# Kernel tuning notes

Measured on AMD Instinct MI355X. Metric: run time of the kernel, lower is better.

## Reference

```python
import jax, jax.numpy as jnp
import numpy as np


def setup_inputs() -> dict:
    key = jax.random.key(0)
    k1, k2 = jax.random.split(key)
    bsz, n_views, d = 4096, 2, 512
    features = jax.random.normal(k1, (bsz, n_views, d), dtype=jnp.float32)
    labels = jax.random.randint(k2, (bsz,), 0, 100)
    return {"features": features, "labels": labels}


def reference(features, labels):
    # Faithful vectorization of Fourdloss.forward (contrast_mode='all').
    bsz, n_views, d = features.shape
    N = bsz * n_views
    # torch.cat(torch.unbind(features, dim=1), dim=0): view-major stacking
    cf = jnp.transpose(features, (1, 0, 2)).reshape(N, d)  # contrast == anchor feature
    lab = jnp.tile(labels, n_views)                        # labels2[i] = labels[i % bsz]
    same = lab[:, None] == lab[None, :]                    # [N, N]
    neg = ~same                                            # mask2
    negf = neg.astype(jnp.float32)
    # positive mask with diagonal removed (mask * logits_mask)
    pos_mask = same.astype(jnp.float32) * (1.0 - jnp.eye(N, dtype=jnp.float32))

    # pairwise dot products with the hardcoded 0.035 temperature
    D = (cf @ cf.T) / 0.035                                # [N, N], D[m, j] = c_m . a_j / 0.035

    # Inner loop over j: over rows m with labels2[m] != labels2[j],
    # S[j] = sum_m exp(D[m, j] - max_m D[m, j])
    maxd = jnp.max(jnp.where(neg, D, -jnp.inf), axis=0)    # [N], per-column masked max
    z = jnp.where(neg, D - maxd[None, :], 0.0)             # safe: masked entries -> exp(0)*0
    S = jnp.sum(jnp.exp(z) * negf, axis=0)                 # [N]

    # Outer loop over i: sum S[j] over all j that are negatives of i; k = count
    num = negf @ S                                         # negtive_dot_negtive_sum
    negcount = negf.sum(axis=1)                            # negtivesum (k)
    x = num / negcount                                     # [N] (repeated across columns in torch)
    log_prob = -jnp.log(x + 1e-12)                         # constant per row

    pos_count = pos_mask.sum(axis=1)
    mask_sum = jnp.where(pos_count == 0, 1.0, pos_count)
    # (mask * log_prob).sum(1) == log_prob * pos_count since log_prob is row-constant
    pos_logits = -(pos_count * log_prob) / mask_sum
    loss = pos_logits.reshape(n_views, bsz).mean()
    return loss
```

## Files before the change

kernel.cpp:

```cpp
#include <hip/hip_runtime.h>

typedef unsigned short u16;
typedef unsigned int u32;
typedef __attribute__((ext_vector_type(8))) short bfrag;
typedef __attribute__((ext_vector_type(4))) float facc;

#define N 8192
#define DIM 512
#define BM 128
#define BK 64
#define NTILE 2080
#define NPART 64
#define NCLS 100

#if __has_builtin(__builtin_amdgcn_exp2f)
#define EXP2(x) __builtin_amdgcn_exp2f(x)
#else
#define EXP2(x) exp2f(x)
#endif

__device__ __forceinline__ u16 f2bf(float f) {
  u32 u = __float_as_uint(f);
  u32 r = u + 0x7fffu + ((u >> 16) & 1u);
  return (u16)(r >> 16);
}
__device__ __forceinline__ float bf2f(u16 h) {
  return __uint_as_float(((u32)h) << 16);
}

__global__ void prep_kernel(const float* __restrict__ F, u16* __restrict__ Ahi,
                            u16* __restrict__ Alo, float* __restrict__ classSum,
                            int* __restrict__ classCnt)
{
  const float sc = sqrtf(1.4426950408889634f / 0.035f);
  int idx = (blockIdx.x * 256 + threadIdx.x) * 4;
  float4 x = *(const float4*)(F + idx);
  float v[4] = {x.x * sc, x.y * sc, x.z * sc, x.w * sc};
  u16 h[4], l[4];
#pragma unroll
  for (int i = 0; i < 4; ++i) {
    h[i] = f2bf(v[i]);
    l[i] = f2bf(v[i] - bf2f(h[i]));
  }
  *(ushort4*)(Ahi + idx) = make_ushort4(h[0], h[1], h[2], h[3]);
  *(ushort4*)(Alo + idx) = make_ushort4(l[0], l[1], l[2], l[3]);
  if (blockIdx.x == 0 && threadIdx.x < NCLS) {
    classSum[threadIdx.x] = 0.f;
    classCnt[threadIdx.x] = 0;
  }
}

__device__ __forceinline__ void stage16(const u16* g, u16* l) {
  __builtin_amdgcn_global_load_lds((const __attribute__((address_space(1))) void*)g,
                                   (__attribute__((address_space(3))) void*)l, 16, 0, 0);
}

__device__ __forceinline__ void mergeMS(float& m, float& s, float m2, float s2) {
  float M = fmaxf(m, m2);
  s = s * EXP2(m - M) + s2 * EXP2(m2 - M);
  m = M;
}

__global__ __launch_bounds__(256, 2) void gram_flash(
    const u16* __restrict__ Ahi, const u16* __restrict__ Alo,
    const int* __restrict__ labels,
    float* __restrict__ m_part, float* __restrict__ s_part)
{
  __shared__ __align__(16) u16 lds[4 * BM * BK];
  u16* lds_ahi = lds;
  u16* lds_alo = lds + BM * BK;
  u16* lds_bhi = lds + 2 * BM * BK;
  u16* lds_blo = lds + 3 * BM * BK;

  const int tid = threadIdx.x;
  const int wave = tid >> 6;
  const int lane = tid & 63;
  const int wr = wave >> 1, wc = wave & 1;
  const int l15 = lane & 15, lg = lane >> 4;

  const int t = blockIdx.x;
  int I = (int)((129.0f - sqrtf(16641.0f - 8.0f * (float)t)) * 0.5f);
  while ((I + 1) * 64 - ((I + 1) * I) / 2 <= t) ++I;
  while (I * 64 - (I * (I - 1)) / 2 > t) --I;
  const int J = I + (t - (I * 64 - (I * (I - 1)) / 2));
  const int i0 = I * BM;
  const int j0 = J * BM;

  u32 lr[4];
#pragma unroll
  for (int mi = 0; mi < 4; ++mi) {
    u32 pk = 0;
#pragma unroll
    for (int rg = 0; rg < 4; ++rg) {
      int r = i0 + wr * 64 + mi * 16 + lg * 4 + rg;
      pk |= ((u32)labels[r >> 1] & 0xffu) << (8 * rg);
    }
    lr[mi] = pk;
  }
  int lc[4];
#pragma unroll
  for (int ni = 0; ni < 4; ++ni)
    lc[ni] = labels[(j0 + wc * 64 + ni * 16 + l15) >> 1];

  facc acc[4][4];
#pragma unroll
  for (int a = 0; a < 4; ++a)
#pragma unroll
    for (int b = 0; b < 4; ++b)
      acc[a][b] = (facc){0.f, 0.f, 0.f, 0.f};

  for (int kk = 0; kk < DIM; kk += BK) {
    __syncthreads();
#pragma unroll
    for (int q = 0; q < 4; ++q) {
      const int ci = (wave * 4 + q) * 64 + lane;
      const int row = ci >> 3;
      const int cp = ci & 7;
      const int cg = cp ^ (row & 7);
      const size_t goffA = (size_t)(i0 + row) * DIM + kk + cg * 8;
      const size_t goffB = (size_t)(j0 + row) * DIM + kk + cg * 8;
      const int lbase = (wave * 4 + q) * 512;
      stage16(Ahi + goffA, lds_ahi + lbase);
      stage16(Alo + goffA, lds_alo + lbase);
      stage16(Ahi + goffB, lds_bhi + lbase);
      stage16(Alo + goffB, lds_blo + lbase);
    }
    asm volatile("s_waitcnt vmcnt(0)" ::: "memory");
    __syncthreads();

#pragma unroll
    for (int k2 = 0; k2 < 2; ++k2) {
      bfrag fah[4], fal[4], fbh[4], fbl[4];
#pragma unroll
      for (int mi = 0; mi < 4; ++mi) {
        const int row = wr * 64 + mi * 16 + l15;
        const int cc = (k2 * 4 + lg) ^ (row & 7);
        const int off = row * 64 + cc * 8;
        fah[mi] = *(const bfrag*)(lds_ahi + off);
        fal[mi] = *(const bfrag*)(lds_alo + off);
      }
#pragma unroll
      for (int ni = 0; ni < 4; ++ni) {
        const int row = wc * 64 + ni * 16 + l15;
        const int cc = (k2 * 4 + lg) ^ (row & 7);
        const int off = row * 64 + cc * 8;
        fbh[ni] = *(const bfrag*)(lds_bhi + off);
        fbl[ni] = *(const bfrag*)(lds_blo + off);
      }
#pragma unroll
      for (int mi = 0; mi < 4; ++mi)
#pragma unroll
        for (int ni = 0; ni < 4; ++ni)
          acc[mi][ni] = __builtin_amdgcn_mfma_f32_16x16x32_bf16(fah[mi], fbh[ni], acc[mi][ni], 0, 0, 0);
#pragma unroll
      for (int mi = 0; mi < 4; ++mi)
#pragma unroll
        for (int ni = 0; ni < 4; ++ni)
          acc[mi][ni] = __builtin_amdgcn_mfma_f32_16x16x32_bf16(fah[mi], fbl[ni], acc[mi][ni], 0, 0, 0);
#pragma unroll
      for (int mi = 0; mi < 4; ++mi)
#pragma unroll
        for (int ni = 0; ni < 4; ++ni)
          acc[mi][ni] = __builtin_amdgcn_mfma_f32_16x16x32_bf16(fal[mi], fbh[ni], acc[mi][ni], 0, 0, 0);
    }
  }

#pragma unroll
  for (int mi = 0; mi < 4; ++mi)
#pragma unroll
    for (int rg = 0; rg < 4; ++rg) {
      const int labr = (int)((lr[mi] >> (8 * rg)) & 0xffu);
#pragma unroll
      for (int ni = 0; ni < 4; ++ni)
        if (labr == lc[ni]) acc[mi][ni][rg] = -1e30f;
    }

  float rm[16], rs[16];
#pragma unroll
  for (int mi = 0; mi < 4; ++mi)
#pragma unroll
    for (int rg = 0; rg < 4; ++rg) {
      const int si = mi * 4 + rg;
      float m = -1e20f;
#pragma unroll
      for (int ni = 0; ni < 4; ++ni) m = fmaxf(m, acc[mi][ni][rg]);
      float s = 0.f;
#pragma unroll
      for (int ni = 0; ni < 4; ++ni) s += EXP2(acc[mi][ni][rg] - m);
      rm[si] = m; rs[si] = s;
    }
#pragma unroll
  for (int st = 1; st <= 8; st <<= 1)
#pragma unroll
    for (int si = 0; si < 16; ++si)
      mergeMS(rm[si], rs[si], __shfl_xor(rm[si], st, 64), __shfl_xor(rs[si], st, 64));

  float cm[4], cs[4];
#pragma unroll
  for (int ni = 0; ni < 4; ++ni) {
    float m = -1e20f;
#pragma unroll
    for (int mi = 0; mi < 4; ++mi)
#pragma unroll
      for (int rg = 0; rg < 4; ++rg) m = fmaxf(m, acc[mi][ni][rg]);
    float s = 0.f;
#pragma unroll
    for (int mi = 0; mi < 4; ++mi)
#pragma unroll
      for (int rg = 0; rg < 4; ++rg) s += EXP2(acc[mi][ni][rg] - m);
    cm[ni] = m; cs[ni] = s;
  }
#pragma unroll
  for (int st = 16; st <= 32; st <<= 1)
#pragma unroll
    for (int ni = 0; ni < 4; ++ni)
      mergeMS(cm[ni], cs[ni], __shfl_xor(cm[ni], st, 64), __shfl_xor(cs[ni], st, 64));

  float* buf = (float*)lds;
  float* RM = buf;
  float* RS = buf + 256;
  float* CM = buf + 512;
  float* CS = buf + 768;

  __syncthreads();
  if (l15 == 0) {
#pragma unroll
    for (int mi = 0; mi < 4; ++mi)
#pragma unroll
      for (int rg = 0; rg < 4; ++rg) {
        const int idx = wr * 64 + mi * 16 + lg * 4 + rg;
        RM[wc * 128 + idx] = rm[mi * 4 + rg];
        RS[wc * 128 + idx] = rs[mi * 4 + rg];
      }
  }
  if (lg == 0 && I != J) {
#pragma unroll
    for (int ni = 0; ni < 4; ++ni) {
      const int c = wc * 64 + ni * 16 + l15;
      CM[wr * 128 + c] = cm[ni];
      CS[wr * 128 + c] = cs[ni];
    }
  }
  __syncthreads();

  if (tid < 128) {
    float m = RM[tid], s = RS[tid];
    mergeMS(m, s, RM[128 + tid], RS[128 + tid]);
    m_part[(size_t)J * N + i0 + tid] = m;
    s_part[(size_t)J * N + i0 + tid] = s;
  } else if (I != J) {
    const int c = tid - 128;
    float m = CM[c], s = CS[c];
    mergeMS(m, s, CM[128 + c], CS[128 + c]);
    m_part[(size_t)I * N + j0 + c] = m;
    s_part[(size_t)I * N + j0 + c] = s;
  }
}

__global__ void combine_kernel(const float* __restrict__ m_part,
                               const float* __restrict__ s_part,
                               const int* __restrict__ labels,
                               float* __restrict__ classSum,
                               int* __restrict__ classCnt)
{
  int j = blockIdx.x * 256 + threadIdx.x;
  float M = -1e20f;
  for (int p = 0; p < NPART; ++p) M = fmaxf(M, m_part[p * N + j]);
  float S = 0.f;
  for (int p = 0; p < NPART; ++p)
    S += s_part[p * N + j] * EXP2(m_part[p * N + j] - M);
  int c = labels[j >> 1];
  atomicAdd(&classSum[c], S);
  atomicAdd(&classCnt[c], 1);
}

__global__ void final_kernel(const float* __restrict__ classSum,
                             const int* __restrict__ classCnt,
                             float* __restrict__ out)
{
  __shared__ float red[128];
  int t = threadIdx.x;
  float total = 0.f;
  for (int c = 0; c < NCLS; ++c) total += classSum[c];
  float term = 0.f;
  if (t < NCLS) {
    int cnt = classCnt[t];
    if (cnt > 0) {
      float x = (total - classSum[t]) / (float)(N - cnt) + 1e-12f;
      term = (float)cnt * logf(x);
    }
  }
  red[t] = term;
  __syncthreads();
  for (int s = 64; s > 0; s >>= 1) {
    if (t < s) red[t] += red[t + s];
    __syncthreads();
  }
  if (t == 0) out[0] = red[0] / (float)N;
}

extern "C" void kernel_launch(void* const* d_in, const int* in_sizes, int n_in,
                              void* d_out, int out_size, void* d_ws, size_t ws_size,
                              hipStream_t stream)
{
  (void)in_sizes; (void)n_in; (void)out_size; (void)ws_size;
  const float* F = (const float*)d_in[0];
  const int* labels = (const int*)d_in[1];
  float* out = (float*)d_out;

  char* ws = (char*)d_ws;
  u16* Ahi = (u16*)ws;
  u16* Alo = (u16*)(ws + (size_t)N * DIM * 2);
  float* m_part = (float*)(ws + (size_t)N * DIM * 4);
  float* s_part = m_part + (size_t)NPART * N;
  float* classSum = s_part + (size_t)NPART * N;
  int* classCnt = (int*)(classSum + NCLS);

  prep_kernel<<<(N * DIM) / 1024, 256, 0, stream>>>(F, Ahi, Alo, classSum, classCnt);
  gram_flash<<<NTILE, 256, 0, stream>>>(Ahi, Alo, labels, m_part, s_part);
  combine_kernel<<<N / 256, 256, 0, stream>>>(m_part, s_part, labels, classSum, classCnt);
  final_kernel<<<1, 128, 0, stream>>>(classSum, classCnt, out);
}
```

Measured before the change: 221.5 us.

## Halve K-tile, raise occupancy, and remap triangular tiles into XCD-local supertiles

The K tile shrinks from 64 to 32, which halves the LDS footprint. Launch bounds are raised to target 4 blocks per CU. The triangular tile index is remapped into 8x8 supertiles, with block IDs interleaved by 8 so that each XCD works on neighbouring tiles and shares their rows in L2. The LDS swizzle is rewritten to pack two rows per 64-element line. The costs are twice as many sync and wait rounds over K and more register pressure under the tighter launch bounds.

```diff
diff --git a/kernel.cpp b/kernel.cpp
--- a/kernel.cpp
+++ b/kernel.cpp
@@ -8,10 +8,11 @@
 #define N 8192
 #define DIM 512
 #define BM 128
-#define BK 64
+#define BK 32
 #define NTILE 2080
 #define NPART 64
 #define NCLS 100
+#define TPX 260
 
 #if __has_builtin(__builtin_amdgcn_exp2f)
 #define EXP2(x) __builtin_amdgcn_exp2f(x)
@@ -61,7 +62,7 @@
   m = M;
 }
 
-__global__ __launch_bounds__(256, 2) void gram_flash(
+__global__ __launch_bounds__(256, 4) void gram_flash(
     const u16* __restrict__ Ahi, const u16* __restrict__ Alo,
     const int* __restrict__ labels,
     float* __restrict__ m_part, float* __restrict__ s_part)
@@ -78,11 +79,27 @@
   const int wr = wave >> 1, wc = wave & 1;
   const int l15 = lane & 15, lg = lane >> 4;
 
-  const int t = blockIdx.x;
-  int I = (int)((129.0f - sqrtf(16641.0f - 8.0f * (float)t)) * 0.5f);
-  while ((I + 1) * 64 - ((I + 1) * I) / 2 <= t) ++I;
-  while (I * 64 - (I * (I - 1)) / 2 > t) --I;
-  const int J = I + (t - (I * 64 - (I * (I - 1)) / 2));
+  const int t = (blockIdx.x & 7) * TPX + (blockIdx.x >> 3);
+  int SI = 0, base = 0;
+  for (;; ++SI) {
+    int rowcnt = 36 + (7 - SI) * 64;
+    if (t < base + rowcnt) break;
+    base += rowcnt;
+  }
+  const int r = t - base;
+  int SJ, li, lj;
+  if (r < 36) {
+    SJ = SI;
+    int a = 0, cum = 0;
+    for (;; ++a) { if (r < cum + (8 - a)) break; cum += 8 - a; }
+    li = a; lj = a + (r - cum);
+  } else {
+    int rr = r - 36;
+    SJ = SI + 1 + (rr >> 6);
+    li = (rr & 63) >> 3;
+    lj = rr & 7;
+  }
+  const int I = SI * 8 + li, J = SJ * 8 + lj;
   const int i0 = I * BM;
   const int j0 = J * BM;
 
@@ -92,8 +109,8 @@
     u32 pk = 0;
 #pragma unroll
     for (int rg = 0; rg < 4; ++rg) {
-      int r = i0 + wr * 64 + mi * 16 + lg * 4 + rg;
-      pk |= ((u32)labels[r >> 1] & 0xffu) << (8 * rg);
+      int rr2 = i0 + wr * 64 + mi * 16 + lg * 4 + rg;
+      pk |= ((u32)labels[rr2 >> 1] & 0xffu) << (8 * rg);
     }
     lr[mi] = pk;
   }
@@ -112,14 +129,16 @@
   for (int kk = 0; kk < DIM; kk += BK) {
     __syncthreads();
 #pragma unroll
-    for (int q = 0; q < 4; ++q) {
-      const int ci = (wave * 4 + q) * 64 + lane;
-      const int row = ci >> 3;
-      const int cp = ci & 7;
-      const int cg = cp ^ (row & 7);
-      const size_t goffA = (size_t)(i0 + row) * DIM + kk + cg * 8;
-      const size_t goffB = (size_t)(j0 + row) * DIM + kk + cg * 8;
-      const int lbase = (wave * 4 + q) * 512;
+    for (int q = 0; q < 2; ++q) {
+      const int ci = (wave * 2 + q) * 64 + lane;
+      const int L = ci >> 3;
+      const int sc2 = ci & 7;
+      const int cb = sc2 ^ (L & 7);
+      const int row = L * 2 + (cb >> 2);
+      const int kc = cb & 3;
+      const size_t goffA = (size_t)(i0 + row) * DIM + kk + kc * 8;
+      const size_t goffB = (size_t)(j0 + row) * DIM + kk + kc * 8;
+      const int lbase = (wave * 2 + q) * 512;
       stage16(Ahi + goffA, lds_ahi + lbase);
       stage16(Alo + goffA, lds_alo + lbase);
       stage16(Ahi + goffB, lds_bhi + lbase);
@@ -128,41 +147,40 @@
     asm volatile("s_waitcnt vmcnt(0)" ::: "memory");
     __syncthreads();
 
-#pragma unroll
-    for (int k2 = 0; k2 < 2; ++k2) {
-      bfrag fah[4], fal[4], fbh[4], fbl[4];
-#pragma unroll
-      for (int mi = 0; mi < 4; ++mi) {
-        const int row = wr * 64 + mi * 16 + l15;
-        const int cc = (k2 * 4 + lg) ^ (row & 7);
-        const int off = row * 64 + cc * 8;
-        fah[mi] = *(const bfrag*)(lds_ahi + off);
-        fal[mi] = *(const bfrag*)(lds_alo + off);
-      }
-#pragma unroll
-      for (int ni = 0; ni < 4; ++ni) {
-        const int row = wc * 64 + ni * 16 + l15;
-        const int cc = (k2 * 4 + lg) ^ (row & 7);
-        const int off = row * 64 + cc * 8;
-        fbh[ni] = *(const bfrag*)(lds_bhi + off);
-        fbl[ni] = *(const bfrag*)(lds_blo + off);
-      }
-#pragma unroll
-      for (int mi = 0; mi < 4; ++mi)
-#pragma unroll
-        for (int ni = 0; ni < 4; ++ni)
-          acc[mi][ni] = __builtin_amdgcn_mfma_f32_16x16x32_bf16(fah[mi], fbh[ni], acc[mi][ni], 0, 0, 0);
-#pragma unroll
-      for (int mi = 0; mi < 4; ++mi)
-#pragma unroll
-        for (int ni = 0; ni < 4; ++ni)
-          acc[mi][ni] = __builtin_amdgcn_mfma_f32_16x16x32_bf16(fah[mi], fbl[ni], acc[mi][ni], 0, 0, 0);
-#pragma unroll
-      for (int mi = 0; mi < 4; ++mi)
-#pragma unroll
-        for (int ni = 0; ni < 4; ++ni)
-          acc[mi][ni] = __builtin_amdgcn_mfma_f32_16x16x32_bf16(fal[mi], fbh[ni], acc[mi][ni], 0, 0, 0);
-    }
+    bfrag fah[4], fal[4], fbh[4], fbl[4];
+#pragma unroll
+    for (int mi = 0; mi < 4; ++mi) {
+      const int row = wr * 64 + mi * 16 + l15;
+      const int L = row >> 1;
+      const int cb = ((row & 1) << 2) | lg;
+      const int off = L * 64 + (cb ^ (L & 7)) * 8;
+      fah[mi] = *(const bfrag*)(lds_ahi + off);
+      fal[mi] = *(const bfrag*)(lds_alo + off);
+    }
+#pragma unroll
+    for (int ni = 0; ni < 4; ++ni) {
+      const int row = wc * 64 + ni * 16 + l15;
+      const int L = row >> 1;
+      const int cb = ((row & 1) << 2) | lg;
+      const int off = L * 64 + (cb ^ (L & 7)) * 8;
+      fbh[ni] = *(const bfrag*)(lds_bhi + off);
+      fbl[ni] = *(const bfrag*)(lds_blo + off);
+    }
+#pragma unroll
+    for (int mi = 0; mi < 4; ++mi)
+#pragma unroll
+      for (int ni = 0; ni < 4; ++ni)
+        acc[mi][ni] = __builtin_amdgcn_mfma_f32_16x16x32_bf16(fah[mi], fbh[ni], acc[mi][ni], 0, 0, 0);
+#pragma unroll
+    for (int mi = 0; mi < 4; ++mi)
+#pragma unroll
+      for (int ni = 0; ni < 4; ++ni)
+        acc[mi][ni] = __builtin_amdgcn_mfma_f32_16x16x32_bf16(fah[mi], fbl[ni], acc[mi][ni], 0, 0, 0);
+#pragma unroll
+    for (int mi = 0; mi < 4; ++mi)
+#pragma unroll
+      for (int ni = 0; ni < 4; ++ni)
+        acc[mi][ni] = __builtin_amdgcn_mfma_f32_16x16x32_bf16(fal[mi], fbh[ni], acc[mi][ni], 0, 0, 0);
   }
 
 #pragma unroll
```

Result: no change. 220.4 us (-0.5%).

## Swizzle triangular tile order into XCD-local supertiles and parallelize combine

Applied to the files above, without the earlier changes.

Remaps the block index of the triangular Gram tile grid so that consecutive blocks on each of the 8 XCDs (blockIdx & 7) walk 8x8 supertiles. Operand row panels then get reused in each XCD's L2 instead of being refetched. The combine kernel now splits the 64 partials across 4 waves per column group, merges them with an online max/sum in shared memory, and launches 4x more blocks for more parallelism. The cost is extra index arithmetic with small loops per block.

```diff
diff --git a/kernel.cpp b/kernel.cpp
--- a/kernel.cpp
+++ b/kernel.cpp
@@ -12,6 +12,7 @@
 #define NTILE 2080
 #define NPART 64
 #define NCLS 100
+#define TPX 260
 
 #if __has_builtin(__builtin_amdgcn_exp2f)
 #define EXP2(x) __builtin_amdgcn_exp2f(x)
@@ -78,11 +79,27 @@
   const int wr = wave >> 1, wc = wave & 1;
   const int l15 = lane & 15, lg = lane >> 4;
 
-  const int t = blockIdx.x;
-  int I = (int)((129.0f - sqrtf(16641.0f - 8.0f * (float)t)) * 0.5f);
-  while ((I + 1) * 64 - ((I + 1) * I) / 2 <= t) ++I;
-  while (I * 64 - (I * (I - 1)) / 2 > t) --I;
-  const int J = I + (t - (I * 64 - (I * (I - 1)) / 2));
+  const int t = (blockIdx.x & 7) * TPX + (blockIdx.x >> 3);
+  int SI = 0, base = 0;
+  for (;; ++SI) {
+    int rowcnt = 36 + (7 - SI) * 64;
+    if (t < base + rowcnt) break;
+    base += rowcnt;
+  }
+  const int r = t - base;
+  int SJ, li, lj;
+  if (r < 36) {
+    SJ = SI;
+    int a = 0, cum = 0;
+    for (;; ++a) { if (r < cum + (8 - a)) break; cum += 8 - a; }
+    li = a; lj = a + (r - cum);
+  } else {
+    int rr = r - 36;
+    SJ = SI + 1 + (rr >> 6);
+    li = (rr & 63) >> 3;
+    lj = rr & 7;
+  }
+  const int I = SI * 8 + li, J = SJ * 8 + lj;
   const int i0 = I * BM;
   const int j0 = J * BM;
 
@@ -92,8 +109,8 @@
     u32 pk = 0;
 #pragma unroll
     for (int rg = 0; rg < 4; ++rg) {
-      int r = i0 + wr * 64 + mi * 16 + lg * 4 + rg;
-      pk |= ((u32)labels[r >> 1] & 0xffu) << (8 * rg);
+      int rr2 = i0 + wr * 64 + mi * 16 + lg * 4 + rg;
+      pk |= ((u32)labels[rr2 >> 1] & 0xffu) << (8 * rg);
     }
     lr[mi] = pk;
   }
@@ -263,15 +280,22 @@
                                float* __restrict__ classSum,
                                int* __restrict__ classCnt)
 {
-  int j = blockIdx.x * 256 + threadIdx.x;
-  float M = -1e20f;
-  for (int p = 0; p < NPART; ++p) M = fmaxf(M, m_part[p * N + j]);
-  float S = 0.f;
-  for (int p = 0; p < NPART; ++p)
-    S += s_part[p * N + j] * EXP2(m_part[p * N + j] - M);
-  int c = labels[j >> 1];
-  atomicAdd(&classSum[c], S);
-  atomicAdd(&classCnt[c], 1);
+  __shared__ float MB[4][64], SB[4][64];
+  const int jloc = threadIdx.x & 63;
+  const int pc = threadIdx.x >> 6;
+  const int j = blockIdx.x * 64 + jloc;
+  float M = -1e20f, S = 0.f;
+  for (int p = pc * 16; p < pc * 16 + 16; ++p)
+    mergeMS(M, S, m_part[(size_t)p * N + j], s_part[(size_t)p * N + j]);
+  MB[pc][jloc] = M; SB[pc][jloc] = S;
+  __syncthreads();
+  if (pc == 0) {
+#pragma unroll
+    for (int q = 1; q < 4; ++q) mergeMS(M, S, MB[q][jloc], SB[q][jloc]);
+    int c = labels[j >> 1];
+    atomicAdd(&classSum[c], S);
+    atomicAdd(&classCnt[c], 1);
+  }
 }
 
 __global__ void final_kernel(const float* __restrict__ classSum,
@@ -318,6 +342,6 @@
 
   prep_kernel<<<(N * DIM) / 1024, 256, 0, stream>>>(F, Ahi, Alo, classSum, classCnt);
   gram_flash<<<NTILE, 256, 0, stream>>>(Ahi, Alo, labels, m_part, s_part);
-  combine_kernel<<<N / 256, 256, 0, stream>>>(m_part, s_part, labels, classSum, classCnt);
+  combine_kernel<<<N / 64, 256, 0, stream>>>(m_part, s_part, labels, classSum, classCnt);
   final_kernel<<<1, 128, 0, stream>>>(classSum, classCnt, out);
 }
```

After: 208.0 us. 6.1% less time.
